# Performance work log

Hardware: AMD Instinct MI355X
Metric: run time of the kernel (lower is better)

## Reference

```python
import jax, jax.numpy as jnp
import numpy as np

HIDDEN = 128
RHO = 5        # K // 2 with K = 10
J = 5
SCALE = 5.0


def setup_inputs() -> dict:
    key = jax.random.key(0)
    ks = jax.random.split(key, 16)
    B, N, D = 2, 4096, HIDDEN
    eigvs = jax.random.uniform(ks[0], (B, N, D), dtype=jnp.float32)  # eigenvalue encodings in [0,1)
    x = jax.random.normal(ks[1], (B, N, D), dtype=jnp.float32)
    U = jax.random.normal(ks[2], (B, N, N), dtype=jnp.float32) / np.sqrt(N)
    s = 1.0 / np.sqrt(D)
    return {
        "eigvs": eigvs, "x": x, "U": U,
        # Linear weights stored as [in, out] (already transposed vs torch)
        "Wa": jax.random.normal(ks[3], (D, RHO), dtype=jnp.float32) * s,
        "ba": jnp.zeros((RHO,), jnp.float32),
        "Wb": jax.random.normal(ks[4], (D, RHO), dtype=jnp.float32) * s,
        "bb": jnp.zeros((RHO,), jnp.float32),
        "Ws": jax.random.normal(ks[5], (D, J), dtype=jnp.float32) * s,
        "bs": jnp.zeros((J,), jnp.float32),
        "WS": jax.random.normal(ks[6], (D, D), dtype=jnp.float32) * s,
        "bS": jnp.zeros((D,), jnp.float32),
        "WM": jax.random.normal(ks[7], (J, D, D), dtype=jnp.float32) * s,
        "bM": jnp.zeros((J, D), jnp.float32),
        "Ww": jax.random.normal(ks[8], (D, D), dtype=jnp.float32) * s,
        "bw": jnp.zeros((D,), jnp.float32),
    }


def _generate_g(a, sx, rho):
    # a: [B, rho]; sx: [B, J, N, D] scaled eigenvalues. Even Chebyshev polys.
    T_odd = jnp.ones_like(sx)
    T_even = sx
    g = a[:, 0, None, None, None] * T_even
    for i in range(1, rho):
        T_odd = 2.0 * sx * T_even - T_odd
        T_even = 2.0 * sx * T_odd - T_even
        g = g + a[:, i, None, None, None] * T_even
    return g


def _generate_h(b, e, rho):
    # b: [B, rho]; e: [B, N, D]. Odd Chebyshev polys.
    T_odd = jnp.ones_like(e)
    T_even = e
    h = b[:, 0, None, None] * T_odd
    for i in range(1, rho):
        T_odd = 2.0 * e * T_even - T_odd
        T_even = 2.0 * e * T_odd - T_even
        h = h + b[:, i, None, None] * T_odd
    return h


def reference(eigvs, x, U, Wa, ba, Wb, bb, Ws, bs, WS, bS, WM, bM, Ww, bw):
    # Filter coefficients from pooled eigenvalue encodings
    a_tilde = (eigvs @ Wa + ba).mean(axis=-2)                      # [B, rho]
    b_tilde = (eigvs @ Wb + bb).mean(axis=-2)                      # [B, rho]
    scale_tilde = jax.nn.sigmoid((eigvs @ Ws + bs).mean(axis=-2)) * SCALE  # [B, J]

    h = _generate_h(b_tilde, eigvs, RHO)                           # [B, N, D] scaling filter
    sx = scale_tilde[:, :, None, None] * eigvs[:, None]            # [B, J, N, D]
    g = _generate_g(a_tilde, sx, RHO)                              # [B, J, N, D] wavelet filters

    # Spectral convolution: U diag(filter) U^T x, per channel
    xt = jnp.einsum('bmn,bmd->bnd', U, x)                          # U^T x
    y_h = jnp.einsum('bnm,bmd->bnd', U, h * xt)                    # [B, N, D]
    y_g = jnp.einsum('bnm,bjmd->bjnd', U, g * xt[:, None])         # [B, J, N, D]

    out = y_h @ WS + bS                                            # S_kernel
    out = out + jnp.einsum('bjnd,jde->bne', y_g, WM) + bM.sum(0)   # sum_j M_kernels[j]
    return out @ Ww + bw                                           # W
```

## Files before the change

kernel.cpp:

```cpp
#include <hip/hip_runtime.h>
#include <hip/hip_bf16.h>
#include <stdint.h>

typedef unsigned short u16;
typedef __attribute__((ext_vector_type(8))) short bf16x8;
typedef __attribute__((ext_vector_type(4))) float f32x4;
typedef __attribute__((ext_vector_type(4))) uint32_t u32x4;

__device__ inline u16 f2bf(float f) {
  union { float f; uint32_t u; } v; v.f = f;
  uint32_t u = v.u;
  u += 0x7FFFu + ((u >> 16) & 1u);
  return (u16)(u >> 16);
}
__device__ inline uint32_t pkbf(float a, float b) {
  union { __hip_bfloat162 h; uint32_t u; } c;
  c.h = __float22bfloat162_rn(float2{a, b});
  return c.u;
}
__device__ inline float bf2f(u16 h) {
  union { uint32_t u; float f; } v; v.u = (uint32_t)h << 16; return v.f;
}
__device__ inline void gl_lds16(const void* g, void* s) {
  __builtin_amdgcn_global_load_lds(
      (const __attribute__((address_space(1))) void*)(uintptr_t)(g),
      (__attribute__((address_space(3))) void*)(uint32_t)(uintptr_t)(s),
      16, 0, 0);
}

__global__ __launch_bounds__(256) void k_pre(
    const float* __restrict__ eig, const float* __restrict__ x,
    const float* __restrict__ WS, const float* __restrict__ WM,
    const float* __restrict__ Ww, const float* __restrict__ bS,
    const float* __restrict__ bM, const float* __restrict__ bw,
    float* __restrict__ part, u16* __restrict__ xT,
    u16* __restrict__ VT, float* __restrict__ cvec) {
  const int bid = blockIdx.x, t = threadIdx.x;
  __shared__ float red[256];
  __shared__ uint32_t L[64][33];
  if (bid < 64) {
    const int b = bid >> 5, chunk = bid & 31;
    const int d = t & 127, half = t >> 7;
    const float* p = eig + ((long)b * 4096 + chunk * 128 + half) * 128 + d;
    float s = 0.0f;
    for (int i = 0; i < 64; i++) s += p[(long)i * 256];
    red[t] = s;
    __syncthreads();
    if (t < 128) part[((long)b * 32 + chunk) * 128 + d] = red[t] + red[t + 128];
    return;
  }
  if (bid < 320) {
    const int q = bid - 64;
    const int b = q >> 7, rem = q & 127;
    const int tr = rem & 63, tc = rem >> 6;
    const float* I = x + (long)b * 524288;
    u16* O = xT + (long)b * 524288;
    const int r = t >> 2, cq = (t & 3) * 4;
    const float* src = I + (long)(tr * 64 + r) * 128 + tc * 64;
#pragma unroll
    for (int i = 0; i < 4; i++) {
      const float4 f = *(const float4*)(src + cq + 16 * i);
      const int c = cq + 16 * i;
      L[r][(c >> 1)]     = pkbf(f.x, f.y);
      L[r][(c >> 1) + 1] = pkbf(f.z, f.w);
    }
    __syncthreads();
    const int r0 = (t & 7) * 8;
#pragma unroll
    for (int p = 0; p < 2; p++) {
      const int c = (t >> 3) + 32 * p;
      uint32_t w[4];
#pragma unroll
      for (int i = 0; i < 4; i++) {
        const uint32_t w0 = L[r0 + 2 * i][c >> 1];
        const uint32_t w1 = L[r0 + 2 * i + 1][c >> 1];
        const u16 v0 = (c & 1) ? (u16)(w0 >> 16) : (u16)(w0 & 0xffff);
        const u16 v1 = (c & 1) ? (u16)(w1 >> 16) : (u16)(w1 & 0xffff);
        w[i] = (uint32_t)v0 | ((uint32_t)v1 << 16);
      }
      u32x4* dst = (u32x4*)(O + (long)(tc * 64 + c) * 4096 + tr * 64 + r0);
      *dst = u32x4{w[0], w[1], w[2], w[3]};
    }
    return;
  }
  if (bid < 704) {
    const int q = (bid - 320) * 2 + (t >> 7);
    const int e = t & 127;
    const int f = q >> 7, d = q & 127;
    const float* Frow = (f == 0) ? (WS + d * 128) : (WM + ((long)(f - 1) * 128 + d) * 128);
    float s = 0.0f;
    for (int k = 0; k < 128; k++) s += Frow[k] * Ww[k * 128 + e];
    VT[(long)e * 768 + f * 128 + d] = f2bf(s);
    return;
  }
  if (t >= 128) return;
  float s = bw[t];
  for (int k = 0; k < 128; k++) {
    float tv = bS[k];
#pragma unroll
    for (int j = 0; j < 5; j++) tv += bM[j * 128 + k];
    s += tv * Ww[k * 128 + t];
  }
  cvec[t] = s;
}

__global__ __launch_bounds__(256) void k_gemm1(
    const u16* __restrict__ xT, const float* __restrict__ U,
    const float* __restrict__ part,
    const float* __restrict__ Wa, const float* __restrict__ ba,
    const float* __restrict__ Wb, const float* __restrict__ bb_,
    const float* __restrict__ Ws, const float* __restrict__ bs,
    float* __restrict__ xs, float* __restrict__ coeff) {
  const int tn = blockIdx.x, ks = blockIdx.y, bb = blockIdx.z;
  const int tid = threadIdx.x;
  __shared__ float sd[128];
  __shared__ __align__(16) u16 As[128 * 32];
  __shared__ __align__(16) u16 Bs[128 * 34 + 64];
  if (tn == 32) {
    if (ks != 0) return;
    if (tid < 128) {
      float s = 0.0f;
      for (int c = 0; c < 32; c++) s += part[((long)bb * 32 + c) * 128 + tid];
      sd[tid] = s * (1.0f / 4096.0f);
    }
    __syncthreads();
    if (tid >= 15) return;
    const int kind = tid / 5, r = tid % 5;
    const float* W = (kind == 0) ? Wa : ((kind == 1) ? Wb : Ws);
    float v = 0.0f;
    for (int d = 0; d < 128; d++) v += sd[d] * W[d * 5 + r];
    v += (kind == 0) ? ba[r] : ((kind == 1) ? bb_[r] : bs[r]);
    if (kind == 2) v = 5.0f / (1.0f + __expf(-v));
    coeff[bb * 16 + kind * 5 + r] = v;
    return;
  }
  const int wave = tid >> 6, lane = tid & 63;
  const int wm = (wave >> 1) * 64, wn = (wave & 1) * 64;
  f32x4 acc[4][4];
#pragma unroll
  for (int i = 0; i < 4; i++)
#pragma unroll
    for (int j = 0; j < 4; j++)
#pragma unroll
      for (int r = 0; r < 4; r++) acc[i][j][r] = 0.0f;
  const int a_off = (wm + (lane & 15)) * 64 + (lane >> 4) * 16;
  const int b_off = (wn + (lane & 15)) * 68 + (lane >> 4) * 16;
  const int srow = wave * 32 + (lane >> 2);
  const int scol = (lane & 3) * 8;
  const u16* Ab = xT + (long)bb * 524288 + ks * 512;
  const int q = tid & 15, cb = tid >> 4;
  const float* Bbase = U + (long)bb * 16777216 + tn * 128 + cb * 8;
  float4 ca0, ca1, cc0, cc1;
  {
    const float* r0 = Bbase + (long)(ks * 512 + 2 * q) * 4096;
    ca0 = *(const float4*)(r0); ca1 = *(const float4*)(r0 + 4);
    const float* r1 = r0 + 4096;
    cc0 = *(const float4*)(r1); cc1 = *(const float4*)(r1 + 4);
  }
  for (int k0 = 0; k0 < 512; k0 += 32) {
#pragma unroll
    for (int i = 0; i < 2; i++)
      gl_lds16(Ab + (long)(srow + i * 16) * 4096 + k0 + scol,
               (char*)As + (wave * 32 + i * 16) * 64);
    {
      uint32_t* dw = (uint32_t*)Bs;
      const int base = (cb * 8) * 17 + q;
      dw[base + 0 * 17] = pkbf(ca0.x, cc0.x);
      dw[base + 1 * 17] = pkbf(ca0.y, cc0.y);
      dw[base + 2 * 17] = pkbf(ca0.z, cc0.z);
      dw[base + 3 * 17] = pkbf(ca0.w, cc0.w);
      dw[base + 4 * 17] = pkbf(ca1.x, cc1.x);
      dw[base + 5 * 17] = pkbf(ca1.y, cc1.y);
      dw[base + 6 * 17] = pkbf(ca1.z, cc1.z);
      dw[base + 7 * 17] = pkbf(ca1.w, cc1.w);
    }
    __syncthreads();
    const int kn = (k0 + 32 < 512) ? (k0 + 32) : k0;
    float4 na0, na1, nc0, nc1;
    {
      const float* r0 = Bbase + (long)(ks * 512 + kn + 2 * q) * 4096;
      na0 = *(const float4*)(r0); na1 = *(const float4*)(r0 + 4);
      const float* r1 = r0 + 4096;
      nc0 = *(const float4*)(r1); nc1 = *(const float4*)(r1 + 4);
    }
    bf16x8 af[4], bfr[4];
#pragma unroll
    for (int mt = 0; mt < 4; mt++)
      af[mt] = *(const bf16x8*)((const char*)As + a_off + mt * 1024);
#pragma unroll
    for (int nt = 0; nt < 4; nt++)
      bfr[nt] = *(const bf16x8*)((const char*)Bs + b_off + nt * 1088);
#pragma unroll
    for (int mt = 0; mt < 4; mt++)
#pragma unroll
      for (int nt = 0; nt < 4; nt++)
        acc[mt][nt] = __builtin_amdgcn_mfma_f32_16x16x32_bf16(af[mt], bfr[nt], acc[mt][nt], 0, 0, 0);
    __syncthreads();
    ca0 = na0; ca1 = na1; cc0 = nc0; cc1 = nc1;
  }
  const int lr = (lane >> 4) * 4, lc = lane & 15;
  float* Cf = xs + (long)bb * 524288 + (long)ks * 1048576;
#pragma unroll
  for (int mt = 0; mt < 4; mt++)
#pragma unroll
    for (int nt = 0; nt < 4; nt++) {
      const int col = tn * 128 + wn + nt * 16 + lc;
#pragma unroll
      for (int r = 0; r < 4; r++) {
        const int row = wm + mt * 16 + lr + r;
        Cf[(long)col * 128 + row] = acc[mt][nt][r];
      }
    }
}

__global__ void k_filter(const float* __restrict__ eig, const float* __restrict__ xs,
                         const float* __restrict__ coeff, u16* __restrict__ Mod) {
  const int b = blockIdx.y;
  const int n = blockIdx.x * 2 + (threadIdx.x >> 7);
  const int d = threadIdx.x & 127;
  const long ridx = (long)b * 4096 + n;
  const long off = ridx * 128 + d;
  const float e = eig[off];
  float xv = 0.0f;
#pragma unroll
  for (int s = 0; s < 8; s++) xv += xs[off + (long)s * 1048576];
  const float* cf = coeff + b * 16;
  float To = 1.0f, Tev = e;
  float h = cf[5];
#pragma unroll
  for (int i = 1; i < 5; i++) {
    To = 2.0f * e * Tev - To;
    Tev = 2.0f * e * To - Tev;
    h += cf[5 + i] * To;
  }
  u16* row = Mod + ridx * 768;
  row[d] = f2bf(h * xv);
#pragma unroll
  for (int j = 0; j < 5; j++) {
    const float sx = cf[10 + j] * e;
    float To2 = 1.0f, Te2 = sx;
    float g = cf[0] * Te2;
#pragma unroll
    for (int i = 1; i < 5; i++) {
      To2 = 2.0f * sx * Te2 - To2;
      Te2 = 2.0f * sx * To2 - Te2;
      g += cf[i] * Te2;
    }
    row[(j + 1) * 128 + d] = f2bf(g * xv);
  }
}

__global__ __launch_bounds__(256) void k_gemm2(
    const u16* __restrict__ VT, const u16* __restrict__ Mod, u16* __restrict__ wT) {
  const int tn = blockIdx.x, bb = blockIdx.z;
  __shared__ __align__(16) u16 As[128 * 32];
  __shared__ __align__(16) u16 Bs[128 * 32];
  const int tid = threadIdx.x, wave = tid >> 6, lane = tid & 63;
  const int wm = (wave >> 1) * 64, wn = (wave & 1) * 64;
  f32x4 acc[4][4];
#pragma unroll
  for (int i = 0; i < 4; i++)
#pragma unroll
    for (int j = 0; j < 4; j++)
#pragma unroll
      for (int r = 0; r < 4; r++) acc[i][j][r] = 0.0f;
  const int a_off = (wm + (lane & 15)) * 64 + (lane >> 4) * 16;
  const int b_off = (wn + (lane & 15)) * 64 + (lane >> 4) * 16;
  const int srow = wave * 32 + (lane >> 2);
  const int scol = (lane & 3) * 8;
  const u16* Bb = Mod + (long)bb * 3145728 + (long)tn * 128 * 768;
  for (int k0 = 0; k0 < 768; k0 += 32) {
#pragma unroll
    for (int i = 0; i < 2; i++) {
      gl_lds16(VT + (long)(srow + i * 16) * 768 + k0 + scol,
               (char*)As + (wave * 32 + i * 16) * 64);
      gl_lds16(Bb + (long)(srow + i * 16) * 768 + k0 + scol,
               (char*)Bs + (wave * 32 + i * 16) * 64);
    }
    __syncthreads();
    bf16x8 af[4], bfr[4];
#pragma unroll
    for (int mt = 0; mt < 4; mt++)
      af[mt] = *(const bf16x8*)((const char*)As + a_off + mt * 1024);
#pragma unroll
    for (int nt = 0; nt < 4; nt++)
      bfr[nt] = *(const bf16x8*)((const char*)Bs + b_off + nt * 1024);
#pragma unroll
    for (int mt = 0; mt < 4; mt++)
#pragma unroll
      for (int nt = 0; nt < 4; nt++)
        acc[mt][nt] = __builtin_amdgcn_mfma_f32_16x16x32_bf16(af[mt], bfr[nt], acc[mt][nt], 0, 0, 0);
    __syncthreads();
  }
  const int lr = (lane >> 4) * 4, lc = lane & 15;
  u16* Cb = wT + (long)bb * 524288;
#pragma unroll
  for (int mt = 0; mt < 4; mt++)
#pragma unroll
    for (int nt = 0; nt < 4; nt++) {
      const int col = tn * 128 + wn + nt * 16 + lc;
#pragma unroll
      for (int r = 0; r < 4; r++) {
        const int row = wm + mt * 16 + lr + r;
        Cb[(long)row * 4096 + col] = f2bf(acc[mt][nt][r]);
      }
    }
}

__global__ __launch_bounds__(256) void k_gemm3(
    const float* __restrict__ U, const u16* __restrict__ wT, u16* __restrict__ os16) {
  const int tm = blockIdx.x, ks = blockIdx.y, bb = blockIdx.z;
  __shared__ __align__(16) u16 As[128 * 32];
  __shared__ __align__(16) u16 Bs[128 * 32];
  const int tid = threadIdx.x, wave = tid >> 6, lane = tid & 63;
  const int wm = (wave >> 1) * 64, wn = (wave & 1) * 64;
  f32x4 acc[4][4];
#pragma unroll
  for (int i = 0; i < 4; i++)
#pragma unroll
    for (int j = 0; j < 4; j++)
#pragma unroll
      for (int r = 0; r < 4; r++) acc[i][j][r] = 0.0f;
  const int a_off = (wm + (lane & 15)) * 64 + (lane >> 4) * 16;
  const int b_off = (wn + (lane & 15)) * 64 + (lane >> 4) * 16;
  const int srow = wave * 32 + (lane >> 2);
  const int scol = (lane & 3) * 8;
  const float* Abase = U + (long)bb * 16777216 +
                       (long)(tm * 128 + (tid >> 2)) * 4096 + (tid & 3) * 8;
  const u16* Bb = wT + (long)bb * 524288 + ks * 512;
  float4 cf0, cf1, cg0, cg1;
  {
    const float* s0 = Abase + ks * 512;
    cf0 = *(const float4*)(s0); cf1 = *(const float4*)(s0 + 4);
    const float* s1 = s0 + 262144;
    cg0 = *(const float4*)(s1); cg1 = *(const float4*)(s1 + 4);
  }
  for (int k0 = 0; k0 < 512; k0 += 32) {
#pragma unroll
    for (int i = 0; i < 2; i++)
      gl_lds16(Bb + (long)(srow + i * 16) * 4096 + k0 + scol,
               (char*)Bs + (wave * 32 + i * 16) * 64);
    *(u32x4*)((char*)As + tid * 16) =
        u32x4{pkbf(cf0.x, cf0.y), pkbf(cf0.z, cf0.w), pkbf(cf1.x, cf1.y), pkbf(cf1.z, cf1.w)};
    *(u32x4*)((char*)As + 4096 + tid * 16) =
        u32x4{pkbf(cg0.x, cg0.y), pkbf(cg0.z, cg0.w), pkbf(cg1.x, cg1.y), pkbf(cg1.z, cg1.w)};
    __syncthreads();
    const int kn = (k0 + 32 < 512) ? (k0 + 32) : k0;
    float4 nf0, nf1, ng0, ng1;
    {
      const float* s0 = Abase + ks * 512 + kn;
      nf0 = *(const float4*)(s0); nf1 = *(const float4*)(s0 + 4);
      const float* s1 = s0 + 262144;
      ng0 = *(const float4*)(s1); ng1 = *(const float4*)(s1 + 4);
    }
    bf16x8 af[4], bfr[4];
#pragma unroll
    for (int mt = 0; mt < 4; mt++)
      af[mt] = *(const bf16x8*)((const char*)As + a_off + mt * 1024);
#pragma unroll
    for (int nt = 0; nt < 4; nt++)
      bfr[nt] = *(const bf16x8*)((const char*)Bs + b_off + nt * 1024);
#pragma unroll
    for (int mt = 0; mt < 4; mt++)
#pragma unroll
      for (int nt = 0; nt < 4; nt++)
        acc[mt][nt] = __builtin_amdgcn_mfma_f32_16x16x32_bf16(af[mt], bfr[nt], acc[mt][nt], 0, 0, 0);
    __syncthreads();
    cf0 = nf0; cf1 = nf1; cg0 = ng0; cg1 = ng1;
  }
  const int lr = (lane >> 4) * 4, lc = lane & 15;
  u16* Cb = os16 + (long)ks * 1048576 + (long)bb * 524288;
#pragma unroll
  for (int mt = 0; mt < 4; mt++)
#pragma unroll
    for (int nt = 0; nt < 4; nt++) {
      const int col = wn + nt * 16 + lc;
#pragma unroll
      for (int r = 0; r < 4; r++) {
        const int row = tm * 128 + wm + mt * 16 + lr + r;
        Cb[(long)row * 128 + col] = f2bf(acc[mt][nt][r]);
      }
    }
}

__global__ void k_outred(const u16* __restrict__ os16, const float* __restrict__ cvec,
                         float* __restrict__ out) {
  const long i = (long)blockIdx.x * 256 + threadIdx.x;
  const long j4 = i * 4;
  float4 r = {0.0f, 0.0f, 0.0f, 0.0f};
#pragma unroll
  for (int s = 0; s < 8; s++) {
    const uint2 v = *(const uint2*)(os16 + j4 + (long)s * 1048576);
    r.x += bf2f((u16)(v.x & 0xffff));
    r.y += bf2f((u16)(v.x >> 16));
    r.z += bf2f((u16)(v.y & 0xffff));
    r.w += bf2f((u16)(v.y >> 16));
  }
  const float4 cv = *(const float4*)(cvec + (i & 31) * 4);
  r.x += cv.x; r.y += cv.y; r.z += cv.z; r.w += cv.w;
  *(float4*)(out + j4) = r;
}

extern "C" void kernel_launch(void* const* d_in, const int* in_sizes, int n_in,
                              void* d_out, int out_size, void* d_ws, size_t ws_size,
                              hipStream_t stream) {
  const float* eig = (const float*)d_in[0];
  const float* x   = (const float*)d_in[1];
  const float* U   = (const float*)d_in[2];
  const float* Wa  = (const float*)d_in[3];
  const float* ba  = (const float*)d_in[4];
  const float* Wb  = (const float*)d_in[5];
  const float* bb  = (const float*)d_in[6];
  const float* Ws  = (const float*)d_in[7];
  const float* bs  = (const float*)d_in[8];
  const float* WSm = (const float*)d_in[9];
  const float* bS  = (const float*)d_in[10];
  const float* WM  = (const float*)d_in[11];
  const float* bM  = (const float*)d_in[12];
  const float* Ww  = (const float*)d_in[13];
  const float* bw  = (const float*)d_in[14];

  char* ws = (char*)d_ws;
  float* xs   = (float*)(ws + 0);
  u16*   os16 = (u16*)(ws + 0);
  u16*   Mod  = (u16*)(ws + 33554432);
  u16*   xT   = (u16*)(ws + 46137344);
  u16*   wT   = (u16*)(ws + 48234496);
  u16*   VT   = (u16*)(ws + 50331648);
  float* part = (float*)(ws + 50528256);
  float* coef = (float*)(ws + 50561024);
  float* cvec = (float*)(ws + 50561152);
  float* outp = (float*)d_out;

  if (ws_size < (size_t)50561664) return;

  k_pre<<<705, 256, 0, stream>>>(eig, x, WSm, WM, Ww, bS, bM, bw, part, xT, VT, cvec);

  k_gemm1<<<dim3(33, 8, 2), 256, 0, stream>>>(xT, U, part, Wa, ba, Wb, bb, Ws, bs, xs, coef);

  k_filter<<<dim3(2048, 2), 256, 0, stream>>>(eig, xs, coef, Mod);

  k_gemm2<<<dim3(32, 1, 2), 256, 0, stream>>>(VT, Mod, wT);

  k_gemm3<<<dim3(32, 8, 2), 256, 0, stream>>>(U, wT, os16);

  k_outred<<<1024, 256, 0, stream>>>(os16, cvec, outp);
}
```

Before: 295.1 us.

## Double-buffer LDS with explicit waitcnt pipelining and XOR swizzle in all three GEMMs

Rewrites the main loops of the three GEMM kernels to use ping-pong LDS buffers. The next tile's global-to-LDS and register prefetch are issued before the current tile's MFMAs, and each step uses a single barrier with hand-placed waitcnt and sched_barrier instead of two syncthreads. It also XOR-swizzles the LDS column slots for the A/B tiles to cut bank conflicts on the bf16x8 reads. This doubles LDS per block, which can lower occupancy, and the hand-written vmcnt counts must match the number of outstanding loads exactly.

```diff
diff --git a/kernel.cpp b/kernel.cpp
--- a/kernel.cpp
+++ b/kernel.cpp
@@ -104,6 +104,7 @@
   cvec[t] = s;
 }
 
+
 __global__ __launch_bounds__(256) void k_gemm1(
     const u16* __restrict__ xT, const float* __restrict__ U,
     const float* __restrict__ part,
@@ -114,8 +115,8 @@
   const int tn = blockIdx.x, ks = blockIdx.y, bb = blockIdx.z;
   const int tid = threadIdx.x;
   __shared__ float sd[128];
-  __shared__ __align__(16) u16 As[128 * 32];
-  __shared__ __align__(16) u16 Bs[128 * 34 + 64];
+  __shared__ __align__(16) u16 As[2 * 128 * 32];
+  __shared__ __align__(16) uint32_t Bsw[2 * 128 * 17];
   if (tn == 32) {
     if (ks != 0) return;
     if (tid < 128) {
@@ -143,61 +144,84 @@
     for (int j = 0; j < 4; j++)
 #pragma unroll
       for (int r = 0; r < 4; r++) acc[i][j][r] = 0.0f;
-  const int a_off = (wm + (lane & 15)) * 64 + (lane >> 4) * 16;
+  const int a_off = (wm + (lane & 15)) * 64 + (((lane >> 4) ^ ((lane >> 1) & 3)) * 16);
   const int b_off = (wn + (lane & 15)) * 68 + (lane >> 4) * 16;
   const int srow = wave * 32 + (lane >> 2);
-  const int scol = (lane & 3) * 8;
+  const int scol_sw = ((lane & 3) ^ ((lane >> 3) & 3)) * 8;
   const u16* Ab = xT + (long)bb * 524288 + ks * 512;
   const int q = tid & 15, cb = tid >> 4;
   const float* Bbase = U + (long)bb * 16777216 + tn * 128 + cb * 8;
-  float4 ca0, ca1, cc0, cc1;
-  {
-    const float* r0 = Bbase + (long)(ks * 512 + 2 * q) * 4096;
-    ca0 = *(const float4*)(r0); ca1 = *(const float4*)(r0 + 4);
-    const float* r1 = r0 + 4096;
-    cc0 = *(const float4*)(r1); cc1 = *(const float4*)(r1 + 4);
-  }
-  for (int k0 = 0; k0 < 512; k0 += 32) {
-#pragma unroll
-    for (int i = 0; i < 2; i++)
-      gl_lds16(Ab + (long)(srow + i * 16) * 4096 + k0 + scol,
-               (char*)As + (wave * 32 + i * 16) * 64);
-    {
-      uint32_t* dw = (uint32_t*)Bs;
-      const int base = (cb * 8) * 17 + q;
-      dw[base + 0 * 17] = pkbf(ca0.x, cc0.x);
-      dw[base + 1 * 17] = pkbf(ca0.y, cc0.y);
-      dw[base + 2 * 17] = pkbf(ca0.z, cc0.z);
-      dw[base + 3 * 17] = pkbf(ca0.w, cc0.w);
-      dw[base + 4 * 17] = pkbf(ca1.x, cc1.x);
-      dw[base + 5 * 17] = pkbf(ca1.y, cc1.y);
-      dw[base + 6 * 17] = pkbf(ca1.z, cc1.z);
-      dw[base + 7 * 17] = pkbf(ca1.w, cc1.w);
-    }
-    __syncthreads();
-    const int kn = (k0 + 32 < 512) ? (k0 + 32) : k0;
-    float4 na0, na1, nc0, nc1;
-    {
-      const float* r0 = Bbase + (long)(ks * 512 + kn + 2 * q) * 4096;
-      na0 = *(const float4*)(r0); na1 = *(const float4*)(r0 + 4);
-      const float* r1 = r0 + 4096;
-      nc0 = *(const float4*)(r1); nc1 = *(const float4*)(r1 + 4);
-    }
-    bf16x8 af[4], bfr[4];
-#pragma unroll
-    for (int mt = 0; mt < 4; mt++)
-      af[mt] = *(const bf16x8*)((const char*)As + a_off + mt * 1024);
-#pragma unroll
-    for (int nt = 0; nt < 4; nt++)
-      bfr[nt] = *(const bf16x8*)((const char*)Bs + b_off + nt * 1088);
-#pragma unroll
-    for (int mt = 0; mt < 4; mt++)
-#pragma unroll
-      for (int nt = 0; nt < 4; nt++)
-        acc[mt][nt] = __builtin_amdgcn_mfma_f32_16x16x32_bf16(af[mt], bfr[nt], acc[mt][nt], 0, 0, 0);
-    __syncthreads();
-    ca0 = na0; ca1 = na1; cc0 = nc0; cc1 = nc1;
-  }
+
+#define G1_STAGEA(KO, BUF) do { \
+    const u16* s_ = Ab + (KO) + scol_sw; \
+    char* d_ = (char*)As + (BUF) * 8192 + wave * 2048; \
+    gl_lds16(s_ + (long)srow * 4096, d_); \
+    gl_lds16(s_ + (long)(srow + 16) * 4096, d_ + 1024); } while (0)
+
+#define G1_LOADB(Pa0, Pa1, Pc0, Pc1, KO) do { \
+    const float* r0_ = Bbase + (long)(ks * 512 + (KO) + 2 * q) * 4096; \
+    Pa0 = *(const float4*)(r0_); Pa1 = *(const float4*)(r0_ + 4); \
+    const float* r1_ = r0_ + 4096; \
+    Pc0 = *(const float4*)(r1_); Pc1 = *(const float4*)(r1_ + 4); } while (0)
+
+#define G1_WRITEB(Pa0, Pa1, Pc0, Pc1, BUF) do { \
+    uint32_t* dw_ = Bsw + (BUF) * 2176 + (cb * 8) * 17 + q; \
+    dw_[0]   = pkbf(Pa0.x, Pc0.x); dw_[17]  = pkbf(Pa0.y, Pc0.y); \
+    dw_[34]  = pkbf(Pa0.z, Pc0.z); dw_[51]  = pkbf(Pa0.w, Pc0.w); \
+    dw_[68]  = pkbf(Pa1.x, Pc1.x); dw_[85]  = pkbf(Pa1.y, Pc1.y); \
+    dw_[102] = pkbf(Pa1.z, Pc1.z); dw_[119] = pkbf(Pa1.w, Pc1.w); } while (0)
+
+#define G1_COMPUTE(BUF) do { \
+    bf16x8 af[4], bfr[4]; \
+    const char* Ab_ = (const char*)As + (BUF) * 8192 + a_off; \
+    const char* Bb_ = (const char*)Bsw + (BUF) * 8704 + b_off; \
+    _Pragma("unroll") for (int mt = 0; mt < 4; mt++) \
+      af[mt] = *(const bf16x8*)(Ab_ + mt * 1024); \
+    _Pragma("unroll") for (int nt = 0; nt < 4; nt++) \
+      bfr[nt] = *(const bf16x8*)(Bb_ + nt * 1088); \
+    _Pragma("unroll") for (int mt = 0; mt < 4; mt++) \
+      _Pragma("unroll") for (int nt = 0; nt < 4; nt++) \
+        acc[mt][nt] = __builtin_amdgcn_mfma_f32_16x16x32_bf16(af[mt], bfr[nt], acc[mt][nt], 0, 0, 0); } while (0)
+
+  float4 pa0, pa1, pc0, pc1;
+  float4 qa0, qa1, qc0, qc1;
+  G1_STAGEA(0, 0);
+  G1_LOADB(pa0, pa1, pc0, pc1, 0);
+  G1_LOADB(qa0, qa1, qc0, qc1, 32);
+  G1_WRITEB(pa0, pa1, pc0, pc1, 0);
+  asm volatile("s_waitcnt vmcnt(0) lgkmcnt(0)" ::: "memory");
+  __builtin_amdgcn_s_barrier();
+  __builtin_amdgcn_sched_barrier(0);
+  for (int it = 0; it < 7; ++it) {
+    const int k0 = it * 64;
+    G1_STAGEA(k0 + 32, 1);
+    __builtin_amdgcn_sched_barrier(0);
+    G1_LOADB(pa0, pa1, pc0, pc1, k0 + 64);
+    G1_COMPUTE(0);
+    G1_WRITEB(qa0, qa1, qc0, qc1, 1);
+    asm volatile("s_waitcnt vmcnt(4) lgkmcnt(0)" ::: "memory");
+    __builtin_amdgcn_s_barrier();
+    __builtin_amdgcn_sched_barrier(0);
+    G1_STAGEA(k0 + 64, 0);
+    __builtin_amdgcn_sched_barrier(0);
+    G1_LOADB(qa0, qa1, qc0, qc1, k0 + 96);
+    G1_COMPUTE(1);
+    G1_WRITEB(pa0, pa1, pc0, pc1, 0);
+    asm volatile("s_waitcnt vmcnt(4) lgkmcnt(0)" ::: "memory");
+    __builtin_amdgcn_s_barrier();
+    __builtin_amdgcn_sched_barrier(0);
+  }
+  G1_STAGEA(480, 1);
+  G1_COMPUTE(0);
+  G1_WRITEB(qa0, qa1, qc0, qc1, 1);
+  asm volatile("s_waitcnt vmcnt(0) lgkmcnt(0)" ::: "memory");
+  __builtin_amdgcn_s_barrier();
+  __builtin_amdgcn_sched_barrier(0);
+  G1_COMPUTE(1);
+#undef G1_STAGEA
+#undef G1_LOADB
+#undef G1_WRITEB
+#undef G1_COMPUTE
   const int lr = (lane >> 4) * 4, lc = lane & 15;
   float* Cf = xs + (long)bb * 524288 + (long)ks * 1048576;
 #pragma unroll
@@ -253,8 +277,8 @@
 __global__ __launch_bounds__(256) void k_gemm2(
     const u16* __restrict__ VT, const u16* __restrict__ Mod, u16* __restrict__ wT) {
   const int tn = blockIdx.x, bb = blockIdx.z;
-  __shared__ __align__(16) u16 As[128 * 32];
-  __shared__ __align__(16) u16 Bs[128 * 32];
+  __shared__ __align__(16) u16 As[2 * 128 * 32];
+  __shared__ __align__(16) u16 Bs[2 * 128 * 32];
   const int tid = threadIdx.x, wave = tid >> 6, lane = tid & 63;
   const int wm = (wave >> 1) * 64, wn = (wave & 1) * 64;
   f32x4 acc[4][4];
@@ -264,34 +288,49 @@
     for (int j = 0; j < 4; j++)
 #pragma unroll
       for (int r = 0; r < 4; r++) acc[i][j][r] = 0.0f;
-  const int a_off = (wm + (lane & 15)) * 64 + (lane >> 4) * 16;
-  const int b_off = (wn + (lane & 15)) * 64 + (lane >> 4) * 16;
+  const int rd_swz = ((lane >> 4) ^ ((lane >> 1) & 3)) * 16;
+  const int a_off = (wm + (lane & 15)) * 64 + rd_swz;
+  const int b_off = (wn + (lane & 15)) * 64 + rd_swz;
   const int srow = wave * 32 + (lane >> 2);
-  const int scol = (lane & 3) * 8;
-  const u16* Bb = Mod + (long)bb * 3145728 + (long)tn * 128 * 768;
-  for (int k0 = 0; k0 < 768; k0 += 32) {
-#pragma unroll
-    for (int i = 0; i < 2; i++) {
-      gl_lds16(VT + (long)(srow + i * 16) * 768 + k0 + scol,
-               (char*)As + (wave * 32 + i * 16) * 64);
-      gl_lds16(Bb + (long)(srow + i * 16) * 768 + k0 + scol,
-               (char*)Bs + (wave * 32 + i * 16) * 64);
-    }
-    __syncthreads();
+  const int scol_sw = ((lane & 3) ^ ((lane >> 3) & 3)) * 8;
+  const u16* Bb = Mod + (long)bb * 3145728 + (long)tn * 98304;
+
+  auto STAGE = [&](int k0, int buf) {
+    char* dA = (char*)As + buf * 8192 + wave * 2048;
+    char* dB = (char*)Bs + buf * 8192 + wave * 2048;
+    gl_lds16(VT + (long)srow * 768 + k0 + scol_sw, dA);
+    gl_lds16(VT + (long)(srow + 16) * 768 + k0 + scol_sw, dA + 1024);
+    gl_lds16(Bb + (long)srow * 768 + k0 + scol_sw, dB);
+    gl_lds16(Bb + (long)(srow + 16) * 768 + k0 + scol_sw, dB + 1024);
+  };
+  auto COMPUTE = [&](int buf) {
     bf16x8 af[4], bfr[4];
-#pragma unroll
-    for (int mt = 0; mt < 4; mt++)
-      af[mt] = *(const bf16x8*)((const char*)As + a_off + mt * 1024);
-#pragma unroll
-    for (int nt = 0; nt < 4; nt++)
-      bfr[nt] = *(const bf16x8*)((const char*)Bs + b_off + nt * 1024);
+    const char* Ab_ = (const char*)As + buf * 8192 + a_off;
+    const char* Bb_ = (const char*)Bs + buf * 8192 + b_off;
+#pragma unroll
+    for (int mt = 0; mt < 4; mt++) af[mt] = *(const bf16x8*)(Ab_ + mt * 1024);
+#pragma unroll
+    for (int nt = 0; nt < 4; nt++) bfr[nt] = *(const bf16x8*)(Bb_ + nt * 1024);
 #pragma unroll
     for (int mt = 0; mt < 4; mt++)
 #pragma unroll
       for (int nt = 0; nt < 4; nt++)
         acc[mt][nt] = __builtin_amdgcn_mfma_f32_16x16x32_bf16(af[mt], bfr[nt], acc[mt][nt], 0, 0, 0);
-    __syncthreads();
-  }
+  };
+
+  STAGE(0, 0);
+  asm volatile("s_waitcnt vmcnt(0)" ::: "memory");
+  __builtin_amdgcn_s_barrier();
+  __builtin_amdgcn_sched_barrier(0);
+  for (int t = 0; t < 23; ++t) {
+    STAGE((t + 1) * 32, (t + 1) & 1);
+    COMPUTE(t & 1);
+    asm volatile("s_waitcnt vmcnt(0) lgkmcnt(0)" ::: "memory");
+    __builtin_amdgcn_s_barrier();
+    __builtin_amdgcn_sched_barrier(0);
+  }
+  COMPUTE(1);
+
   const int lr = (lane >> 4) * 4, lc = lane & 15;
   u16* Cb = wT + (long)bb * 524288;
 #pragma unroll
@@ -310,8 +349,8 @@
 __global__ __launch_bounds__(256) void k_gemm3(
     const float* __restrict__ U, const u16* __restrict__ wT, u16* __restrict__ os16) {
   const int tm = blockIdx.x, ks = blockIdx.y, bb = blockIdx.z;
-  __shared__ __align__(16) u16 As[128 * 32];
-  __shared__ __align__(16) u16 Bs[128 * 32];
+  __shared__ __align__(16) u16 As[2 * 128 * 32];
+  __shared__ __align__(16) u16 Bs[2 * 128 * 32];
   const int tid = threadIdx.x, wave = tid >> 6, lane = tid & 63;
   const int wm = (wave >> 1) * 64, wn = (wave & 1) * 64;
   f32x4 acc[4][4];
@@ -321,53 +360,86 @@
     for (int j = 0; j < 4; j++)
 #pragma unroll
       for (int r = 0; r < 4; r++) acc[i][j][r] = 0.0f;
-  const int a_off = (wm + (lane & 15)) * 64 + (lane >> 4) * 16;
-  const int b_off = (wn + (lane & 15)) * 64 + (lane >> 4) * 16;
+  const int rd_swz = ((lane >> 4) ^ ((lane >> 1) & 3)) * 16;
+  const int a_off = (wm + (lane & 15)) * 64 + rd_swz;
+  const int b_off = (wn + (lane & 15)) * 64 + rd_swz;
   const int srow = wave * 32 + (lane >> 2);
-  const int scol = (lane & 3) * 8;
+  const int scol_sw = ((lane & 3) ^ ((lane >> 3) & 3)) * 8;
+  const int wslot = ((tid & 3) ^ ((tid >> 3) & 3));
   const float* Abase = U + (long)bb * 16777216 +
                        (long)(tm * 128 + (tid >> 2)) * 4096 + (tid & 3) * 8;
   const u16* Bb = wT + (long)bb * 524288 + ks * 512;
-  float4 cf0, cf1, cg0, cg1;
-  {
-    const float* s0 = Abase + ks * 512;
-    cf0 = *(const float4*)(s0); cf1 = *(const float4*)(s0 + 4);
-    const float* s1 = s0 + 262144;
-    cg0 = *(const float4*)(s1); cg1 = *(const float4*)(s1 + 4);
-  }
-  for (int k0 = 0; k0 < 512; k0 += 32) {
-#pragma unroll
-    for (int i = 0; i < 2; i++)
-      gl_lds16(Bb + (long)(srow + i * 16) * 4096 + k0 + scol,
-               (char*)Bs + (wave * 32 + i * 16) * 64);
-    *(u32x4*)((char*)As + tid * 16) =
-        u32x4{pkbf(cf0.x, cf0.y), pkbf(cf0.z, cf0.w), pkbf(cf1.x, cf1.y), pkbf(cf1.z, cf1.w)};
-    *(u32x4*)((char*)As + 4096 + tid * 16) =
-        u32x4{pkbf(cg0.x, cg0.y), pkbf(cg0.z, cg0.w), pkbf(cg1.x, cg1.y), pkbf(cg1.z, cg1.w)};
-    __syncthreads();
-    const int kn = (k0 + 32 < 512) ? (k0 + 32) : k0;
-    float4 nf0, nf1, ng0, ng1;
-    {
-      const float* s0 = Abase + ks * 512 + kn;
-      nf0 = *(const float4*)(s0); nf1 = *(const float4*)(s0 + 4);
-      const float* s1 = s0 + 262144;
-      ng0 = *(const float4*)(s1); ng1 = *(const float4*)(s1 + 4);
-    }
-    bf16x8 af[4], bfr[4];
-#pragma unroll
-    for (int mt = 0; mt < 4; mt++)
-      af[mt] = *(const bf16x8*)((const char*)As + a_off + mt * 1024);
-#pragma unroll
-    for (int nt = 0; nt < 4; nt++)
-      bfr[nt] = *(const bf16x8*)((const char*)Bs + b_off + nt * 1024);
-#pragma unroll
-    for (int mt = 0; mt < 4; mt++)
-#pragma unroll
-      for (int nt = 0; nt < 4; nt++)
-        acc[mt][nt] = __builtin_amdgcn_mfma_f32_16x16x32_bf16(af[mt], bfr[nt], acc[mt][nt], 0, 0, 0);
-    __syncthreads();
-    cf0 = nf0; cf1 = nf1; cg0 = ng0; cg1 = ng1;
-  }
+
+#define G3_STAGEB(KO, BUF) do { \
+    const u16* s_ = Bb + (KO) + scol_sw; \
+    char* d_ = (char*)Bs + (BUF) * 8192 + wave * 2048; \
+    gl_lds16(s_ + (long)srow * 4096, d_); \
+    gl_lds16(s_ + (long)(srow + 16) * 4096, d_ + 1024); } while (0)
+
+#define G3_LOADA(Pf0, Pf1, Pg0, Pg1, KO) do { \
+    const float* s0_ = Abase + ks * 512 + (KO); \
+    Pf0 = *(const float4*)(s0_); Pf1 = *(const float4*)(s0_ + 4); \
+    const float* s1_ = s0_ + 262144; \
+    Pg0 = *(const float4*)(s1_); Pg1 = *(const float4*)(s1_ + 4); } while (0)
+
+#define G3_WRITEA(Pf0, Pf1, Pg0, Pg1, BUF) do { \
+    char* d_ = (char*)As + (BUF) * 8192 + (tid >> 2) * 64 + wslot * 16; \
+    *(u32x4*)(d_) = u32x4{pkbf(Pf0.x, Pf0.y), pkbf(Pf0.z, Pf0.w), \
+                          pkbf(Pf1.x, Pf1.y), pkbf(Pf1.z, Pf1.w)}; \
+    *(u32x4*)(d_ + 4096) = u32x4{pkbf(Pg0.x, Pg0.y), pkbf(Pg0.z, Pg0.w), \
+                                 pkbf(Pg1.x, Pg1.y), pkbf(Pg1.z, Pg1.w)}; } while (0)
+
+#define G3_COMPUTE(BUF) do { \
+    bf16x8 af[4], bfr[4]; \
+    const char* Ab_ = (const char*)As + (BUF) * 8192 + a_off; \
+    const char* Bb_ = (const char*)Bs + (BUF) * 8192 + b_off; \
+    _Pragma("unroll") for (int mt = 0; mt < 4; mt++) \
+      af[mt] = *(const bf16x8*)(Ab_ + mt * 1024); \
+    _Pragma("unroll") for (int nt = 0; nt < 4; nt++) \
+      bfr[nt] = *(const bf16x8*)(Bb_ + nt * 1024); \
+    _Pragma("unroll") for (int mt = 0; mt < 4; mt++) \
+      _Pragma("unroll") for (int nt = 0; nt < 4; nt++) \
+        acc[mt][nt] = __builtin_amdgcn_mfma_f32_16x16x32_bf16(af[mt], bfr[nt], acc[mt][nt], 0, 0, 0); } while (0)
+
+  float4 pf0, pf1, pg0, pg1;
+  float4 qf0, qf1, qg0, qg1;
+  G3_STAGEB(0, 0);
+  G3_LOADA(pf0, pf1, pg0, pg1, 0);
+  G3_LOADA(qf0, qf1, qg0, qg1, 32);
+  G3_WRITEA(pf0, pf1, pg0, pg1, 0);
+  asm volatile("s_waitcnt vmcnt(0) lgkmcnt(0)" ::: "memory");
+  __builtin_amdgcn_s_barrier();
+  __builtin_amdgcn_sched_barrier(0);
+  for (int it = 0; it < 7; ++it) {
+    const int k0 = it * 64;
+    G3_STAGEB(k0 + 32, 1);
+    __builtin_amdgcn_sched_barrier(0);
+    G3_LOADA(pf0, pf1, pg0, pg1, k0 + 64);
+    G3_COMPUTE(0);
+    G3_WRITEA(qf0, qf1, qg0, qg1, 1);
+    asm volatile("s_waitcnt vmcnt(4) lgkmcnt(0)" ::: "memory");
+    __builtin_amdgcn_s_barrier();
+    __builtin_amdgcn_sched_barrier(0);
+    G3_STAGEB(k0 + 64, 0);
+    __builtin_amdgcn_sched_barrier(0);
+    G3_LOADA(qf0, qf1, qg0, qg1, k0 + 96);
+    G3_COMPUTE(1);
+    G3_WRITEA(pf0, pf1, pg0, pg1, 0);
+    asm volatile("s_waitcnt vmcnt(4) lgkmcnt(0)" ::: "memory");
+    __builtin_amdgcn_s_barrier();
+    __builtin_amdgcn_sched_barrier(0);
+  }
+  G3_STAGEB(480, 1);
+  G3_COMPUTE(0);
+  G3_WRITEA(qf0, qf1, qg0, qg1, 1);
+  asm volatile("s_waitcnt vmcnt(0) lgkmcnt(0)" ::: "memory");
+  __builtin_amdgcn_s_barrier();
+  __builtin_amdgcn_sched_barrier(0);
+  G3_COMPUTE(1);
+#undef G3_STAGEB
+#undef G3_LOADA
+#undef G3_WRITEA
+#undef G3_COMPUTE
   const int lr = (lane >> 4) * 4, lc = lane & 15;
   u16* Cb = os16 + (long)ks * 1048576 + (long)bb * 524288;
 #pragma unroll
```

New measurement: 296.3 us. Within noise of the previous version (+0.4%).

## Pre-convert U to bf16 and transpose, triple-buffer GEMMs with async LDS loads

Applied to the files above, without the earlier changes.

k_pre gains 8192 extra blocks that convert U to bf16 and also write a transposed bf16 copy. All three GEMMs then stream both operands straight into LDS through global_load_lds with an XOR swizzle, using a three-stage buffer and raw waitcnt/barrier scheduling in place of register prefetch plus __syncthreads. This removes the per-iteration fp32 loads, the packing and the strided transposed reads of U inside the GEMMs. In exchange it adds a full read of U (2x64MB fp32) and writes of 2x32MB bf16 copies every call, and it needs a much larger workspace.

```diff
diff --git a/kernel.cpp b/kernel.cpp
--- a/kernel.cpp
+++ b/kernel.cpp
@@ -30,11 +30,13 @@
 
 __global__ __launch_bounds__(256) void k_pre(
     const float* __restrict__ eig, const float* __restrict__ x,
+    const float* __restrict__ U,
     const float* __restrict__ WS, const float* __restrict__ WM,
     const float* __restrict__ Ww, const float* __restrict__ bS,
     const float* __restrict__ bM, const float* __restrict__ bw,
     float* __restrict__ part, u16* __restrict__ xT,
-    u16* __restrict__ VT, float* __restrict__ cvec) {
+    u16* __restrict__ VT, float* __restrict__ cvec,
+    u16* __restrict__ Ubf, u16* __restrict__ UTr) {
   const int bid = blockIdx.x, t = threadIdx.x;
   __shared__ float red[256];
   __shared__ uint32_t L[64][33];
@@ -93,19 +95,59 @@
     VT[(long)e * 768 + f * 128 + d] = f2bf(s);
     return;
   }
-  if (t >= 128) return;
-  float s = bw[t];
-  for (int k = 0; k < 128; k++) {
-    float tv = bS[k];
-#pragma unroll
-    for (int j = 0; j < 5; j++) tv += bM[j * 128 + k];
-    s += tv * Ww[k * 128 + t];
-  }
-  cvec[t] = s;
-}
+  if (bid == 704) {
+    if (t >= 128) return;
+    float s = bw[t];
+    for (int k = 0; k < 128; k++) {
+      float tv = bS[k];
+#pragma unroll
+      for (int j = 0; j < 5; j++) tv += bM[j * 128 + k];
+      s += tv * Ww[k * 128 + t];
+    }
+    cvec[t] = s;
+    return;
+  }
+  {
+    const int q = bid - 705;
+    const int b = q >> 12, rem = q & 4095;
+    const int ti = rem & 63, tj = rem >> 6;
+    const float* Iu = U + (long)b * 16777216 + (long)ti * 64 * 4096 + tj * 64;
+    u16* Ou = Ubf + (long)b * 16777216 + (long)ti * 64 * 4096 + tj * 64;
+    u16* Ot = UTr + (long)b * 16777216 + (long)tj * 64 * 4096 + ti * 64;
+    const int r = t >> 2, cq = (t & 3) * 4;
+    const float* src = Iu + (long)r * 4096 + cq;
+    u16* dstS = Ou + (long)r * 4096 + cq;
+#pragma unroll
+    for (int i = 0; i < 4; i++) {
+      const float4 f = *(const float4*)(src + 16 * i);
+      const int c = cq + 16 * i;
+      *(uint2*)(dstS + 16 * i) = uint2{pkbf(f.x, f.y), pkbf(f.z, f.w)};
+      L[r][(c >> 1)]     = pkbf(f.x, f.y);
+      L[r][(c >> 1) + 1] = pkbf(f.z, f.w);
+    }
+    __syncthreads();
+    const int r0 = (t & 7) * 8;
+#pragma unroll
+    for (int p = 0; p < 2; p++) {
+      const int c = (t >> 3) + 32 * p;
+      uint32_t w[4];
+#pragma unroll
+      for (int i = 0; i < 4; i++) {
+        const uint32_t w0 = L[r0 + 2 * i][c >> 1];
+        const uint32_t w1 = L[r0 + 2 * i + 1][c >> 1];
+        const u16 v0 = (c & 1) ? (u16)(w0 >> 16) : (u16)(w0 & 0xffff);
+        const u16 v1 = (c & 1) ? (u16)(w1 >> 16) : (u16)(w1 & 0xffff);
+        w[i] = (uint32_t)v0 | ((uint32_t)v1 << 16);
+      }
+      u32x4* dst = (u32x4*)(Ot + (long)c * 4096 + r0);
+      *dst = u32x4{w[0], w[1], w[2], w[3]};
+    }
+  }
+}
+
 
 __global__ __launch_bounds__(256) void k_gemm1(
-    const u16* __restrict__ xT, const float* __restrict__ U,
+    const u16* __restrict__ xT, const u16* __restrict__ UTr,
     const float* __restrict__ part,
     const float* __restrict__ Wa, const float* __restrict__ ba,
     const float* __restrict__ Wb, const float* __restrict__ bb_,
@@ -114,8 +156,8 @@
   const int tn = blockIdx.x, ks = blockIdx.y, bb = blockIdx.z;
   const int tid = threadIdx.x;
   __shared__ float sd[128];
-  __shared__ __align__(16) u16 As[128 * 32];
-  __shared__ __align__(16) u16 Bs[128 * 34 + 64];
+  __shared__ __align__(16) u16 As[3 * 4096];
+  __shared__ __align__(16) u16 Bs[3 * 4096];
   if (tn == 32) {
     if (ks != 0) return;
     if (tid < 128) {
@@ -143,61 +185,56 @@
     for (int j = 0; j < 4; j++)
 #pragma unroll
       for (int r = 0; r < 4; r++) acc[i][j][r] = 0.0f;
-  const int a_off = (wm + (lane & 15)) * 64 + (lane >> 4) * 16;
-  const int b_off = (wn + (lane & 15)) * 68 + (lane >> 4) * 16;
+  const int swz_rd = ((lane >> 4) ^ ((lane >> 1) & 3)) * 16;
+  const int a_off = (wm + (lane & 15)) * 64 + swz_rd;
+  const int b_off = (wn + (lane & 15)) * 64 + swz_rd;
   const int srow = wave * 32 + (lane >> 2);
-  const int scol = (lane & 3) * 8;
-  const u16* Ab = xT + (long)bb * 524288 + ks * 512;
-  const int q = tid & 15, cb = tid >> 4;
-  const float* Bbase = U + (long)bb * 16777216 + tn * 128 + cb * 8;
-  float4 ca0, ca1, cc0, cc1;
-  {
-    const float* r0 = Bbase + (long)(ks * 512 + 2 * q) * 4096;
-    ca0 = *(const float4*)(r0); ca1 = *(const float4*)(r0 + 4);
-    const float* r1 = r0 + 4096;
-    cc0 = *(const float4*)(r1); cc1 = *(const float4*)(r1 + 4);
-  }
-  for (int k0 = 0; k0 < 512; k0 += 32) {
-#pragma unroll
-    for (int i = 0; i < 2; i++)
-      gl_lds16(Ab + (long)(srow + i * 16) * 4096 + k0 + scol,
-               (char*)As + (wave * 32 + i * 16) * 64);
-    {
-      uint32_t* dw = (uint32_t*)Bs;
-      const int base = (cb * 8) * 17 + q;
-      dw[base + 0 * 17] = pkbf(ca0.x, cc0.x);
-      dw[base + 1 * 17] = pkbf(ca0.y, cc0.y);
-      dw[base + 2 * 17] = pkbf(ca0.z, cc0.z);
-      dw[base + 3 * 17] = pkbf(ca0.w, cc0.w);
-      dw[base + 4 * 17] = pkbf(ca1.x, cc1.x);
-      dw[base + 5 * 17] = pkbf(ca1.y, cc1.y);
-      dw[base + 6 * 17] = pkbf(ca1.z, cc1.z);
-      dw[base + 7 * 17] = pkbf(ca1.w, cc1.w);
-    }
-    __syncthreads();
-    const int kn = (k0 + 32 < 512) ? (k0 + 32) : k0;
-    float4 na0, na1, nc0, nc1;
-    {
-      const float* r0 = Bbase + (long)(ks * 512 + kn + 2 * q) * 4096;
-      na0 = *(const float4*)(r0); na1 = *(const float4*)(r0 + 4);
-      const float* r1 = r0 + 4096;
-      nc0 = *(const float4*)(r1); nc1 = *(const float4*)(r1 + 4);
-    }
+  const int scol = ((lane & 3) ^ ((lane >> 3) & 3)) * 8;
+  const u16* Asrc = xT + (long)bb * 524288 + ks * 512 + scol;
+  const u16* Bsrc = UTr + (long)bb * 16777216 + (long)tn * 524288 + ks * 512 + scol;
+
+  auto STAGE = [&](int k0, int buf) {
+    char* dA = (char*)As + buf * 8192 + wave * 2048;
+    char* dB = (char*)Bs + buf * 8192 + wave * 2048;
+    gl_lds16(Asrc + (long)srow * 4096 + k0, dA);
+    gl_lds16(Asrc + (long)(srow + 16) * 4096 + k0, dA + 1024);
+    gl_lds16(Bsrc + (long)srow * 4096 + k0, dB);
+    gl_lds16(Bsrc + (long)(srow + 16) * 4096 + k0, dB + 1024);
+  };
+  auto COMPUTE = [&](int buf) {
     bf16x8 af[4], bfr[4];
-#pragma unroll
-    for (int mt = 0; mt < 4; mt++)
-      af[mt] = *(const bf16x8*)((const char*)As + a_off + mt * 1024);
-#pragma unroll
-    for (int nt = 0; nt < 4; nt++)
-      bfr[nt] = *(const bf16x8*)((const char*)Bs + b_off + nt * 1088);
+    const char* Ab_ = (const char*)As + buf * 8192 + a_off;
+    const char* Bb_ = (const char*)Bs + buf * 8192 + b_off;
+#pragma unroll
+    for (int mt = 0; mt < 4; mt++) af[mt] = *(const bf16x8*)(Ab_ + mt * 1024);
+#pragma unroll
+    for (int nt = 0; nt < 4; nt++) bfr[nt] = *(const bf16x8*)(Bb_ + nt * 1024);
 #pragma unroll
     for (int mt = 0; mt < 4; mt++)
 #pragma unroll
       for (int nt = 0; nt < 4; nt++)
         acc[mt][nt] = __builtin_amdgcn_mfma_f32_16x16x32_bf16(af[mt], bfr[nt], acc[mt][nt], 0, 0, 0);
-    __syncthreads();
-    ca0 = na0; ca1 = na1; cc0 = nc0; cc1 = nc1;
-  }
+  };
+
+  STAGE(0, 0);
+  STAGE(32, 1);
+  asm volatile("s_waitcnt vmcnt(4)" ::: "memory");
+  __builtin_amdgcn_s_barrier();
+  __builtin_amdgcn_sched_barrier(0);
+#pragma unroll
+  for (int t = 0; t < 14; ++t) {
+    STAGE((t + 2) * 32, (t + 2) % 3);
+    COMPUTE(t % 3);
+    asm volatile("s_waitcnt vmcnt(4)" ::: "memory");
+    __builtin_amdgcn_s_barrier();
+    __builtin_amdgcn_sched_barrier(0);
+  }
+  COMPUTE(2);
+  asm volatile("s_waitcnt vmcnt(0)" ::: "memory");
+  __builtin_amdgcn_s_barrier();
+  __builtin_amdgcn_sched_barrier(0);
+  COMPUTE(0);
+
   const int lr = (lane >> 4) * 4, lc = lane & 15;
   float* Cf = xs + (long)bb * 524288 + (long)ks * 1048576;
 #pragma unroll
@@ -253,8 +290,8 @@
 __global__ __launch_bounds__(256) void k_gemm2(
     const u16* __restrict__ VT, const u16* __restrict__ Mod, u16* __restrict__ wT) {
   const int tn = blockIdx.x, bb = blockIdx.z;
-  __shared__ __align__(16) u16 As[128 * 32];
-  __shared__ __align__(16) u16 Bs[128 * 32];
+  __shared__ __align__(16) u16 As[3 * 4096];
+  __shared__ __align__(16) u16 Bs[3 * 4096];
   const int tid = threadIdx.x, wave = tid >> 6, lane = tid & 63;
   const int wm = (wave >> 1) * 64, wn = (wave & 1) * 64;
   f32x4 acc[4][4];
@@ -264,34 +301,56 @@
     for (int j = 0; j < 4; j++)
 #pragma unroll
       for (int r = 0; r < 4; r++) acc[i][j][r] = 0.0f;
-  const int a_off = (wm + (lane & 15)) * 64 + (lane >> 4) * 16;
-  const int b_off = (wn + (lane & 15)) * 64 + (lane >> 4) * 16;
+  const int swz_rd = ((lane >> 4) ^ ((lane >> 1) & 3)) * 16;
+  const int a_off = (wm + (lane & 15)) * 64 + swz_rd;
+  const int b_off = (wn + (lane & 15)) * 64 + swz_rd;
   const int srow = wave * 32 + (lane >> 2);
-  const int scol = (lane & 3) * 8;
-  const u16* Bb = Mod + (long)bb * 3145728 + (long)tn * 128 * 768;
-  for (int k0 = 0; k0 < 768; k0 += 32) {
-#pragma unroll
-    for (int i = 0; i < 2; i++) {
-      gl_lds16(VT + (long)(srow + i * 16) * 768 + k0 + scol,
-               (char*)As + (wave * 32 + i * 16) * 64);
-      gl_lds16(Bb + (long)(srow + i * 16) * 768 + k0 + scol,
-               (char*)Bs + (wave * 32 + i * 16) * 64);
-    }
-    __syncthreads();
+  const int scol = ((lane & 3) ^ ((lane >> 3) & 3)) * 8;
+  const u16* Asrc = VT + scol;
+  const u16* Bsrc = Mod + (long)bb * 3145728 + (long)tn * 98304 + scol;
+
+  auto STAGE = [&](int k0, int buf) {
+    char* dA = (char*)As + buf * 8192 + wave * 2048;
+    char* dB = (char*)Bs + buf * 8192 + wave * 2048;
+    gl_lds16(Asrc + (long)srow * 768 + k0, dA);
+    gl_lds16(Asrc + (long)(srow + 16) * 768 + k0, dA + 1024);
+    gl_lds16(Bsrc + (long)srow * 768 + k0, dB);
+    gl_lds16(Bsrc + (long)(srow + 16) * 768 + k0, dB + 1024);
+  };
+  auto COMPUTE = [&](int buf) {
     bf16x8 af[4], bfr[4];
-#pragma unroll
-    for (int mt = 0; mt < 4; mt++)
-      af[mt] = *(const bf16x8*)((const char*)As + a_off + mt * 1024);
-#pragma unroll
-    for (int nt = 0; nt < 4; nt++)
-      bfr[nt] = *(const bf16x8*)((const char*)Bs + b_off + nt * 1024);
+    const char* Ab_ = (const char*)As + buf * 8192 + a_off;
+    const char* Bb_ = (const char*)Bs + buf * 8192 + b_off;
+#pragma unroll
+    for (int mt = 0; mt < 4; mt++) af[mt] = *(const bf16x8*)(Ab_ + mt * 1024);
+#pragma unroll
+    for (int nt = 0; nt < 4; nt++) bfr[nt] = *(const bf16x8*)(Bb_ + nt * 1024);
 #pragma unroll
     for (int mt = 0; mt < 4; mt++)
 #pragma unroll
       for (int nt = 0; nt < 4; nt++)
         acc[mt][nt] = __builtin_amdgcn_mfma_f32_16x16x32_bf16(af[mt], bfr[nt], acc[mt][nt], 0, 0, 0);
-    __syncthreads();
-  }
+  };
+
+  STAGE(0, 0);
+  STAGE(32, 1);
+  asm volatile("s_waitcnt vmcnt(4)" ::: "memory");
+  __builtin_amdgcn_s_barrier();
+  __builtin_amdgcn_sched_barrier(0);
+#pragma unroll
+  for (int t = 0; t < 22; ++t) {
+    STAGE((t + 2) * 32, (t + 2) % 3);
+    COMPUTE(t % 3);
+    asm volatile("s_waitcnt vmcnt(4)" ::: "memory");
+    __builtin_amdgcn_s_barrier();
+    __builtin_amdgcn_sched_barrier(0);
+  }
+  COMPUTE(1);
+  asm volatile("s_waitcnt vmcnt(0)" ::: "memory");
+  __builtin_amdgcn_s_barrier();
+  __builtin_amdgcn_sched_barrier(0);
+  COMPUTE(2);
+
   const int lr = (lane >> 4) * 4, lc = lane & 15;
   u16* Cb = wT + (long)bb * 524288;
 #pragma unroll
@@ -308,10 +367,10 @@
 }
 
 __global__ __launch_bounds__(256) void k_gemm3(
-    const float* __restrict__ U, const u16* __restrict__ wT, u16* __restrict__ os16) {
+    const u16* __restrict__ Ubf, const u16* __restrict__ wT, u16* __restrict__ os16) {
   const int tm = blockIdx.x, ks = blockIdx.y, bb = blockIdx.z;
-  __shared__ __align__(16) u16 As[128 * 32];
-  __shared__ __align__(16) u16 Bs[128 * 32];
+  __shared__ __align__(16) u16 As[3 * 4096];
+  __shared__ __align__(16) u16 Bs[3 * 4096];
   const int tid = threadIdx.x, wave = tid >> 6, lane = tid & 63;
   const int wm = (wave >> 1) * 64, wn = (wave & 1) * 64;
   f32x4 acc[4][4];
@@ -321,53 +380,56 @@
     for (int j = 0; j < 4; j++)
 #pragma unroll
       for (int r = 0; r < 4; r++) acc[i][j][r] = 0.0f;
-  const int a_off = (wm + (lane & 15)) * 64 + (lane >> 4) * 16;
-  const int b_off = (wn + (lane & 15)) * 64 + (lane >> 4) * 16;
+  const int swz_rd = ((lane >> 4) ^ ((lane >> 1) & 3)) * 16;
+  const int a_off = (wm + (lane & 15)) * 64 + swz_rd;
+  const int b_off = (wn + (lane & 15)) * 64 + swz_rd;
   const int srow = wave * 32 + (lane >> 2);
-  const int scol = (lane & 3) * 8;
-  const float* Abase = U + (long)bb * 16777216 +
-                       (long)(tm * 128 + (tid >> 2)) * 4096 + (tid & 3) * 8;
-  const u16* Bb = wT + (long)bb * 524288 + ks * 512;
-  float4 cf0, cf1, cg0, cg1;
-  {
-    const float* s0 = Abase + ks * 512;
-    cf0 = *(const float4*)(s0); cf1 = *(const float4*)(s0 + 4);
-    const float* s1 = s0 + 262144;
-    cg0 = *(const float4*)(s1); cg1 = *(const float4*)(s1 + 4);
-  }
-  for (int k0 = 0; k0 < 512; k0 += 32) {
-#pragma unroll
-    for (int i = 0; i < 2; i++)
-      gl_lds16(Bb + (long)(srow + i * 16) * 4096 + k0 + scol,
-               (char*)Bs + (wave * 32 + i * 16) * 64);
-    *(u32x4*)((char*)As + tid * 16) =
-        u32x4{pkbf(cf0.x, cf0.y), pkbf(cf0.z, cf0.w), pkbf(cf1.x, cf1.y), pkbf(cf1.z, cf1.w)};
-    *(u32x4*)((char*)As + 4096 + tid * 16) =
-        u32x4{pkbf(cg0.x, cg0.y), pkbf(cg0.z, cg0.w), pkbf(cg1.x, cg1.y), pkbf(cg1.z, cg1.w)};
-    __syncthreads();
-    const int kn = (k0 + 32 < 512) ? (k0 + 32) : k0;
-    float4 nf0, nf1, ng0, ng1;
-    {
-      const float* s0 = Abase + ks * 512 + kn;
-      nf0 = *(const float4*)(s0); nf1 = *(const float4*)(s0 + 4);
-      const float* s1 = s0 + 262144;
-      ng0 = *(const float4*)(s1); ng1 = *(const float4*)(s1 + 4);
-    }
+  const int scol = ((lane & 3) ^ ((lane >> 3) & 3)) * 8;
+  const u16* Asrc = Ubf + (long)bb * 16777216 + (long)tm * 524288 + ks * 512 + scol;
+  const u16* Bsrc = wT + (long)bb * 524288 + ks * 512 + scol;
+
+  auto STAGE = [&](int k0, int buf) {
+    char* dA = (char*)As + buf * 8192 + wave * 2048;
+    char* dB = (char*)Bs + buf * 8192 + wave * 2048;
+    gl_lds16(Asrc + (long)srow * 4096 + k0, dA);
+    gl_lds16(Asrc + (long)(srow + 16) * 4096 + k0, dA + 1024);
+    gl_lds16(Bsrc + (long)srow * 4096 + k0, dB);
+    gl_lds16(Bsrc + (long)(srow + 16) * 4096 + k0, dB + 1024);
+  };
+  auto COMPUTE = [&](int buf) {
     bf16x8 af[4], bfr[4];
-#pragma unroll
-    for (int mt = 0; mt < 4; mt++)
-      af[mt] = *(const bf16x8*)((const char*)As + a_off + mt * 1024);
-#pragma unroll
-    for (int nt = 0; nt < 4; nt++)
-      bfr[nt] = *(const bf16x8*)((const char*)Bs + b_off + nt * 1024);
+    const char* Ab_ = (const char*)As + buf * 8192 + a_off;
+    const char* Bb_ = (const char*)Bs + buf * 8192 + b_off;
+#pragma unroll
+    for (int mt = 0; mt < 4; mt++) af[mt] = *(const bf16x8*)(Ab_ + mt * 1024);
+#pragma unroll
+    for (int nt = 0; nt < 4; nt++) bfr[nt] = *(const bf16x8*)(Bb_ + nt * 1024);
 #pragma unroll
     for (int mt = 0; mt < 4; mt++)
 #pragma unroll
       for (int nt = 0; nt < 4; nt++)
         acc[mt][nt] = __builtin_amdgcn_mfma_f32_16x16x32_bf16(af[mt], bfr[nt], acc[mt][nt], 0, 0, 0);
-    __syncthreads();
-    cf0 = nf0; cf1 = nf1; cg0 = ng0; cg1 = ng1;
-  }
+  };
+
+  STAGE(0, 0);
+  STAGE(32, 1);
+  asm volatile("s_waitcnt vmcnt(4)" ::: "memory");
+  __builtin_amdgcn_s_barrier();
+  __builtin_amdgcn_sched_barrier(0);
+#pragma unroll
+  for (int t = 0; t < 14; ++t) {
+    STAGE((t + 2) * 32, (t + 2) % 3);
+    COMPUTE(t % 3);
+    asm volatile("s_waitcnt vmcnt(4)" ::: "memory");
+    __builtin_amdgcn_s_barrier();
+    __builtin_amdgcn_sched_barrier(0);
+  }
+  COMPUTE(2);
+  asm volatile("s_waitcnt vmcnt(0)" ::: "memory");
+  __builtin_amdgcn_s_barrier();
+  __builtin_amdgcn_sched_barrier(0);
+  COMPUTE(0);
+
   const int lr = (lane >> 4) * 4, lc = lane & 15;
   u16* Cb = os16 + (long)ks * 1048576 + (long)bb * 524288;
 #pragma unroll
@@ -430,19 +492,22 @@
   float* part = (float*)(ws + 50528256);
   float* coef = (float*)(ws + 50561024);
   float* cvec = (float*)(ws + 50561152);
+  u16*   Ubf  = (u16*)(ws + 52428800);
+  u16*   UTr  = (u16*)(ws + 119537664);
   float* outp = (float*)d_out;
 
-  if (ws_size < (size_t)50561664) return;
-
-  k_pre<<<705, 256, 0, stream>>>(eig, x, WSm, WM, Ww, bS, bM, bw, part, xT, VT, cvec);
-
-  k_gemm1<<<dim3(33, 8, 2), 256, 0, stream>>>(xT, U, part, Wa, ba, Wb, bb, Ws, bs, xs, coef);
+  if (ws_size < (size_t)186646528) return;
+
+  k_pre<<<8897, 256, 0, stream>>>(eig, x, U, WSm, WM, Ww, bS, bM, bw,
+                                  part, xT, VT, cvec, Ubf, UTr);
+
+  k_gemm1<<<dim3(33, 8, 2), 256, 0, stream>>>(xT, UTr, part, Wa, ba, Wb, bb, Ws, bs, xs, coef);
 
   k_filter<<<dim3(2048, 2), 256, 0, stream>>>(eig, xs, coef, Mod);
 
   k_gemm2<<<dim3(32, 1, 2), 256, 0, stream>>>(VT, Mod, wT);
 
-  k_gemm3<<<dim3(32, 8, 2), 256, 0, stream>>>(U, wT, os16);
+  k_gemm3<<<dim3(32, 8, 2), 256, 0, stream>>>(Ubf, wT, os16);
 
   k_outred<<<1024, 256, 0, stream>>>(os16, cvec, outp);
 }
```

Measured after the change: 329.3 us. 1.12x slower.
